# Kernel tuning notes

Measured on AMD Instinct MI355X. Metric: run time of the kernel, lower is better.

Reference implementation:

```python
import jax, jax.numpy as jnp
import numpy as np

N_NODES = 50000
N_EDGES = 800000
FEAT_DIM = 64
NUM_RELS = 8


def setup_inputs() -> dict:
    key = jax.random.key(0)
    k1, k2, k3, k4, k5 = jax.random.split(key, 5)
    features = jax.random.normal(k1, (N_NODES, FEAT_DIM), dtype=jnp.float32)
    # xavier_uniform with relu gain ~= sqrt(2)*sqrt(6/(D+D))
    limit = np.sqrt(2.0) * np.sqrt(6.0 / (FEAT_DIM + FEAT_DIM))
    weight_r = jax.random.uniform(k2, (NUM_RELS, FEAT_DIM, FEAT_DIM), dtype=jnp.float32,
                                  minval=-limit, maxval=limit)
    src = jax.random.randint(k3, (N_EDGES,), 0, N_NODES, dtype=jnp.int64 if jax.config.jax_enable_x64 else jnp.int32)
    dst = jax.random.randint(k4, (N_EDGES,), 0, N_NODES, dtype=src.dtype)
    etype = jax.random.randint(k5, (N_EDGES,), 0, NUM_RELS, dtype=src.dtype)
    return {"features": features, "weight_r": weight_r, "src": src, "dst": dst, "etype": etype}


def reference(features, weight_r, src, dst, etype):
    N, D = features.shape
    c = 0.2
    # in-degree of each destination node (DGL 'deg' node data)
    deg = jax.ops.segment_sum(jnp.ones(dst.shape, dtype=features.dtype), dst, num_segments=N)
    # relation-batched matmul: h @ W_r for every relation, then gather per edge.
    # [R, N, D] = 8*50000*64 floats -- cheap vs. materializing [E, D, D] weights.
    hw = jnp.einsum('nd,rdf->rnf', features, weight_r)
    msg = hw[etype, src] / deg[dst][:, None]          # [E, D]
    M = jax.ops.segment_sum(msg, dst, num_segments=N)  # scatter-sum mailbox reduce
    updated = jax.nn.relu(c * features + (1.0 - c) * M)
    # DGL only applies reduce to nodes that received messages; others keep h.
    return jnp.where((deg > 0)[:, None], updated, features)
```

## Files before the change

### kernel.cpp

```cpp
#include <hip/hip_runtime.h>
#include <hip/hip_bf16.h>

#define N_NODES 50000
#define N_EDGES 800000
#define FEAT 64
#define NRELS 8
#define NPB 32
#define NBUCK 1563
#define NBP 196
#define BCAP 768
#define FB_BLOCKS 782

typedef __attribute__((ext_vector_type(8))) short bf16x8;
typedef __attribute__((ext_vector_type(4))) float f32x4;

static __host__ __device__ inline size_t align256(size_t x) { return (x + 255) & ~(size_t)255; }

__device__ inline unsigned short f2b(float f) {
    unsigned u = __builtin_bit_cast(unsigned, f);
    unsigned r = (u + 0x7fffu + ((u >> 16) & 1u)) >> 16;
    return (unsigned short)r;
}
__device__ inline float b2f(unsigned short u) {
    unsigned v = ((unsigned)u) << 16;
    return __builtin_bit_cast(float, v);
}

__global__ void bfill_kernel(const int* __restrict__ dst, const int* __restrict__ srcv,
                             const int* __restrict__ et, const float* __restrict__ W,
                             const float* __restrict__ feat,
                             int* __restrict__ bcnt, int* __restrict__ tmp,
                             unsigned short* __restrict__ WtT,
                             unsigned short* __restrict__ Fb, int E, int N) {
    const int t = threadIdx.x;

    if (blockIdx.x >= NBP) {
        const int fbb = blockIdx.x - NBP;
        if (fbb < 32) {
            int i4 = fbb * 256 + t;
            float4 v = ((const float4*)W)[i4];
            int bse = i4 * 4;
            int f0 = bse & 63;
            int rd = bse >> 6;
            int d  = rd & 63;
            int r  = rd >> 6;
            unsigned short* w0 = WtT + ((size_t)(r * 64 + f0) * 64 + d);
            w0[0 * 64] = f2b(v.x);
            w0[1 * 64] = f2b(v.y);
            w0[2 * 64] = f2b(v.z);
            w0[3 * 64] = f2b(v.w);
        }
        const int node = fbb * 64 + (t >> 2);
        if (node >= N) return;
        const int seg = t & 3;
        const float4* F4 = (const float4*)feat + (size_t)node * 16 + seg * 4;
        float4 v0 = F4[0], v1 = F4[1], v2 = F4[2], v3 = F4[3];
        bf16x8 b0, b1;
        b0[0] = (short)f2b(v0.x); b0[1] = (short)f2b(v0.y);
        b0[2] = (short)f2b(v0.z); b0[3] = (short)f2b(v0.w);
        b0[4] = (short)f2b(v1.x); b0[5] = (short)f2b(v1.y);
        b0[6] = (short)f2b(v1.z); b0[7] = (short)f2b(v1.w);
        b1[0] = (short)f2b(v2.x); b1[1] = (short)f2b(v2.y);
        b1[2] = (short)f2b(v2.z); b1[3] = (short)f2b(v2.w);
        b1[4] = (short)f2b(v3.x); b1[5] = (short)f2b(v3.y);
        b1[6] = (short)f2b(v3.z); b1[7] = (short)f2b(v3.w);
        *(bf16x8*)(Fb + (size_t)node * 64 + seg * 16)     = b0;
        *(bf16x8*)(Fb + (size_t)node * 64 + seg * 16 + 8) = b1;
        return;
    }

    __shared__ int hist[NBUCK];
    __shared__ int base[NBUCK];
    __shared__ int lcur[NBUCK];
    for (int j = t; j < NBUCK; j += 256) { hist[j] = 0; lcur[j] = 0; }
    __syncthreads();

    const int4* dst4 = (const int4*)dst;
    const int4* src4 = (const int4*)srcv;
    const int4* et4  = (const int4*)et;
    const int n4 = E >> 2;
    int bk[16], pk[16];
#pragma unroll
    for (int k = 0; k < 4; k++) {
        int i4 = blockIdx.x * 1024 + t + k * 256;
        if (i4 < n4) {
            int4 d = dst4[i4];
            int4 s = src4[i4];
            int4 r = et4[i4];
            const int dd[4] = {d.x, d.y, d.z, d.w};
            const int ss[4] = {s.x, s.y, s.z, s.w};
            const int rr[4] = {r.x, r.y, r.z, r.w};
#pragma unroll
            for (int j = 0; j < 4; j++) {
                int idx = k * 4 + j;
                bk[idx] = dd[j] >> 5;
                pk[idx] = (ss[j] & 0xFFFF) | (rr[j] << 16) | ((dd[j] & 31) << 19);
                atomicAdd(&hist[bk[idx]], 1);
            }
        } else {
#pragma unroll
            for (int j = 0; j < 4; j++) bk[k * 4 + j] = -1;
        }
    }
    __syncthreads();
    for (int j = t; j < NBUCK; j += 256)
        if (hist[j] > 0)
            base[j] = j * BCAP + atomicAdd(&bcnt[j], hist[j]);
    __syncthreads();
#pragma unroll
    for (int k = 0; k < 16; k++) {
        if (bk[k] >= 0) {
            int r = atomicAdd(&lcur[bk[k]], 1);
            int pos = base[bk[k]] + r;
            if (pos < (bk[k] + 1) * BCAP)
                tmp[pos] = pk[k];
        }
    }
}

__global__ __launch_bounds__(256, 4) void fuse_kernel(
    const int* __restrict__ bcnt, const int* __restrict__ tmp,
    const unsigned short* __restrict__ Fb,
    const unsigned short* __restrict__ WtT, const float* __restrict__ feat,
    float* __restrict__ out, int N) {
    __shared__ unsigned short Sb[NRELS][NPB][64];
    __shared__ int sedge[BCAP];
    __shared__ int hist[256];
    __shared__ int noff[NPB + 1];
    __shared__ int wsum[4];
    const int t = threadIdx.x;
    const int bkt = blockIdx.x;
    const int n0 = bkt * NPB;
    const int nn = min(NPB, N - n0);
    const int gid = t >> 3, q = t & 7;

    {
        f32x4 z = {0.f, 0.f, 0.f, 0.f};
        f32x4* zp = (f32x4*)&Sb[0][0][0];
#pragma unroll
        for (int i = 0; i < 8; i++) zp[t + 256 * i] = z;
    }
    hist[t] = 0;
    __syncthreads();

    const int cnt = min(bcnt[bkt], BCAP);
    const int* tb = tmp + (size_t)bkt * BCAP;
    int v0 = (t < cnt) ? tb[t] : -1;
    int v1 = (t + 256 < cnt) ? tb[t + 256] : -1;
    int v2 = (t + 512 < cnt) ? tb[t + 512] : -1;
    if (v0 >= 0) atomicAdd(&hist[(v0 >> 16) & 255], 1);
    if (v1 >= 0) atomicAdd(&hist[(v1 >> 16) & 255], 1);
    if (v2 >= 0) atomicAdd(&hist[(v2 >> 16) & 255], 1);
    __syncthreads();
    const int myc = hist[t];
    int x = myc;
#pragma unroll
    for (int o = 1; o < 64; o <<= 1) {
        int u_ = __shfl_up(x, o);
        if ((t & 63) >= o) x += u_;
    }
    if ((t & 63) == 63) wsum[t >> 6] = x;
    __syncthreads();
    {
        int add = 0;
        const int wv = t >> 6;
        if (wv > 0) add += wsum[0];
        if (wv > 1) add += wsum[1];
        if (wv > 2) add += wsum[2];
        x += add;
    }
    const int ex = x - myc;
    if ((t & 7) == 0) noff[t >> 3] = ex;
    if (t == 255) noff[NPB] = ex + myc;
    hist[t] = ex;
    __syncthreads();
    if (v0 >= 0) { int p = atomicAdd(&hist[(v0 >> 16) & 255], 1); sedge[p] = v0; }
    if (v1 >= 0) { int p = atomicAdd(&hist[(v1 >> 16) & 255], 1); sedge[p] = v1; }
    if (v2 >= 0) { int p = atomicAdd(&hist[(v2 >> 16) & 255], 1); sedge[p] = v2; }
    __syncthreads();

    int b = 0, e = 0;
    if (gid < nn) { b = noff[gid]; e = noff[gid + 1]; }
    if (gid < nn && b < e) {
        const int swz = (q ^ (gid & 7)) * 8;
        unsigned short* srow = &Sb[0][0][0] + (size_t)gid * 64 + swz;
        float a[8] = {0.f, 0.f, 0.f, 0.f, 0.f, 0.f, 0.f, 0.f};
        int curR = -1;

        auto flushS = [&](int rel) {
            bf16x8 v;
#pragma unroll
            for (int k = 0; k < 8; k++) v[k] = (short)f2b(a[k]);
            *(bf16x8*)(srow + (size_t)rel * (NPB * 64)) = v;
        };

        int pkc[2][8];
        bf16x8 uc[2][8];
#pragma unroll
        for (int j = 0; j < 8; j++) {
            int pk = (b + j < e) ? sedge[b + j] : -1;
            pkc[0][j] = pk;
            uc[0][j] = (bf16x8){0, 0, 0, 0, 0, 0, 0, 0};
            if (pk >= 0)
                uc[0][j] = *(const bf16x8*)(Fb + (size_t)(pk & 0xFFFF) * 64 + q * 8);
        }
        __builtin_amdgcn_sched_barrier(0);
#pragma unroll
        for (int c = 0; c < 4; c++) {
            const int cur = c & 1, nxt = (c & 1) ^ 1;
            if (c < 3) {
                const int cb = b + (c + 1) * 8;
#pragma unroll
                for (int j = 0; j < 8; j++) {
                    int pk = (cb + j < e) ? sedge[cb + j] : -1;
                    pkc[nxt][j] = pk;
                    uc[nxt][j] = (bf16x8){0, 0, 0, 0, 0, 0, 0, 0};
                    if (pk >= 0)
                        uc[nxt][j] = *(const bf16x8*)(Fb + (size_t)(pk & 0xFFFF) * 64 + q * 8);
                }
            }
            __builtin_amdgcn_sched_barrier(0);
#pragma unroll
            for (int j = 0; j < 8; j++) {
                int pk = pkc[cur][j];
                if (pk >= 0) {
                    bf16x8 uu = uc[cur][j];
                    int rel = (pk >> 16) & 7;
                    if (rel != curR) {
                        if (curR >= 0) flushS(curR);
                        curR = rel;
#pragma unroll
                        for (int k = 0; k < 8; k++) a[k] = b2f((unsigned short)uu[k]);
                    } else {
#pragma unroll
                        for (int k = 0; k < 8; k++) a[k] += b2f((unsigned short)uu[k]);
                    }
                }
            }
            if (b + (c + 1) * 8 >= e) break;
        }
        for (int i = b + 32; i < e; i++) {
            int pk = sedge[i];
            bf16x8 uu = *(const bf16x8*)(Fb + (size_t)(pk & 0xFFFF) * 64 + q * 8);
            int rel = (pk >> 16) & 7;
            if (rel != curR) {
                if (curR >= 0) flushS(curR);
                curR = rel;
#pragma unroll
                for (int k = 0; k < 8; k++) a[k] = b2f((unsigned short)uu[k]);
            } else {
#pragma unroll
                for (int k = 0; k < 8; k++) a[k] += b2f((unsigned short)uu[k]);
            }
        }
        if (curR >= 0) flushS(curR);
    }

    float4 h0e = make_float4(0.f, 0.f, 0.f, 0.f), h1e = h0e;
    const int ef0 = q * 8;
    if (gid < nn) {
        const float4* fp = (const float4*)feat + (size_t)(n0 + gid) * 16 + (ef0 >> 2);
        h0e = fp[0];
        h1e = fp[1];
    }
    __syncthreads();

    const int w = t >> 6, l = t & 63, col = l & 15, quad = l >> 4;
    f32x4 acc0 = {0.f, 0.f, 0.f, 0.f}, acc1 = {0.f, 0.f, 0.f, 0.f};
    const int sw0 = (quad ^ (col & 7)) * 8;
    const int sw1 = ((quad + 4) ^ (col & 7)) * 8;
#pragma unroll
    for (int r = 0; r < NRELS; r++) {
        const unsigned short* wp = WtT + (size_t)r * 4096 + ((w * 16 + col) * 64 + quad * 8);
        bf16x8 b0 = *(const bf16x8*)wp;
        bf16x8 b1 = *(const bf16x8*)(wp + 32);
        const unsigned short* Sr = &Sb[0][0][0] + (size_t)r * (NPB * 64);
        bf16x8 a0 = *(const bf16x8*)&Sr[col * 64 + sw0];
        bf16x8 a1 = *(const bf16x8*)&Sr[col * 64 + sw1];
        bf16x8 c0 = *(const bf16x8*)&Sr[(16 + col) * 64 + sw0];
        bf16x8 c1 = *(const bf16x8*)&Sr[(16 + col) * 64 + sw1];
        acc0 = __builtin_amdgcn_mfma_f32_16x16x32_bf16(a0, b0, acc0, 0, 0, 0);
        acc0 = __builtin_amdgcn_mfma_f32_16x16x32_bf16(a1, b1, acc0, 0, 0, 0);
        acc1 = __builtin_amdgcn_mfma_f32_16x16x32_bf16(c0, b0, acc1, 0, 0, 0);
        acc1 = __builtin_amdgcn_mfma_f32_16x16x32_bf16(c1, b1, acc1, 0, 0, 0);
    }
    __syncthreads();

    float* C = (float*)&Sb[0][0][0];
#pragma unroll
    for (int i = 0; i < 4; i++) {
        C[(quad * 4 + i) * 72 + w * 16 + col]        = acc0[i];
        C[(16 + quad * 4 + i) * 72 + w * 16 + col]   = acc1[i];
    }
    __syncthreads();

    if (gid < nn) {
        const int gn = n0 + gid;
        const int deg = e - b;
        float4 m0 = *(const float4*)&C[gid * 72 + ef0];
        float4 m1 = *(const float4*)&C[gid * 72 + ef0 + 4];
        float4 r0, r1;
        if (deg > 0) {
            float inv = 0.8f / (float)deg;
            r0.x = fmaxf(0.2f * h0e.x + m0.x * inv, 0.f);
            r0.y = fmaxf(0.2f * h0e.y + m0.y * inv, 0.f);
            r0.z = fmaxf(0.2f * h0e.z + m0.z * inv, 0.f);
            r0.w = fmaxf(0.2f * h0e.w + m0.w * inv, 0.f);
            r1.x = fmaxf(0.2f * h1e.x + m1.x * inv, 0.f);
            r1.y = fmaxf(0.2f * h1e.y + m1.y * inv, 0.f);
            r1.z = fmaxf(0.2f * h1e.z + m1.z * inv, 0.f);
            r1.w = fmaxf(0.2f * h1e.w + m1.w * inv, 0.f);
        } else {
            r0 = h0e; r1 = h1e;
        }
        float4* op = (float4*)out + (size_t)gn * 16 + (ef0 >> 2);
        op[0] = r0;
        op[1] = r1;
    }
}

__global__ void degf_kernel(const int* __restrict__ dst, float* __restrict__ deg, int E) {
    int e = blockIdx.x * blockDim.x + threadIdx.x;
    if (e < E) atomicAdd(deg + dst[e], 1.0f);
}

__global__ void otf_kernel(const int* __restrict__ src, const int* __restrict__ dst,
                           const int* __restrict__ et, const float* __restrict__ feat,
                           const float* __restrict__ W, float* __restrict__ out, int E) {
    int wid = (blockIdx.x * blockDim.x + threadIdx.x) >> 6;
    int l = threadIdx.x & 63;
    if (wid >= E) return;
    int s = src[wid], dd = dst[wid], r = et[wid];
    float fv = feat[(size_t)s * 64 + l];
    const float* Wr = W + (size_t)r * 4096;
    float acc = 0.f;
#pragma unroll
    for (int d = 0; d < 64; d++) {
        float a = __shfl(fv, d);
        acc += a * Wr[d * 64 + l];
    }
    atomicAdd(out + (size_t)dd * 64 + l, acc);
}

__global__ void final_kernel(const float* __restrict__ feat, const float* __restrict__ deg,
                             float* __restrict__ out, int N) {
    int i = blockIdx.x * blockDim.x + threadIdx.x;
    if (i >= N * 16) return;
    int n = i >> 4;
    float d = deg[n];
    float4 f = ((const float4*)feat)[i];
    float4 m = ((float4*)out)[i];
    float4 res;
    if (d > 0.f) {
        float inv = 0.8f / d;
        res.x = fmaxf(0.2f * f.x + m.x * inv, 0.f);
        res.y = fmaxf(0.2f * f.y + m.y * inv, 0.f);
        res.z = fmaxf(0.2f * f.z + m.z * inv, 0.f);
        res.w = fmaxf(0.2f * f.w + m.w * inv, 0.f);
    } else {
        res = f;
    }
    ((float4*)out)[i] = res;
}

extern "C" void kernel_launch(void* const* d_in, const int* in_sizes, int n_in,
                              void* d_out, int out_size, void* d_ws, size_t ws_size,
                              hipStream_t stream) {
    const float* feat = (const float*)d_in[0];
    const float* W    = (const float*)d_in[1];
    const int*   src  = (const int*)d_in[2];
    const int*   dst  = (const int*)d_in[3];
    const int*   et   = (const int*)d_in[4];
    float* out = (float*)d_out;

    const int N = N_NODES, E = N_EDGES;

    char* p = (char*)d_ws;
    int* bcnt  = (int*)p;  p += align256((size_t)NBUCK * 4);
    int* tmp   = (int*)p;  p += align256((size_t)NBUCK * BCAP * 4);
    unsigned short* WtT = (unsigned short*)p;
    p += align256((size_t)NRELS * FEAT * FEAT * 2);
    unsigned short* Fb = (unsigned short*)p;
    p += align256((size_t)N * FEAT * 2);
    size_t need_full = (size_t)(p - (char*)d_ws);

    if (ws_size >= need_full) {
        hipMemsetAsync(bcnt, 0, (size_t)NBUCK * 4, stream);
        bfill_kernel<<<NBP + FB_BLOCKS, 256, 0, stream>>>(dst, src, et, W, feat,
                                                          bcnt, tmp, WtT, Fb, E, N);
        fuse_kernel<<<NBUCK, 256, 0, stream>>>(bcnt, tmp, Fb, WtT, feat, out, N);
    } else {
        float* deg = (float*)d_ws;
        hipMemsetAsync(out, 0, (size_t)N * FEAT * 4, stream);
        hipMemsetAsync(deg, 0, (size_t)N * 4, stream);
        degf_kernel<<<(E + 255) / 256, 256, 0, stream>>>(dst, deg, E);
        otf_kernel<<<(E + 3) / 4, 256, 0, stream>>>(src, dst, et, feat, W, out, E);
        final_kernel<<<(N * 16 + 255) / 256, 256, 0, stream>>>(feat, deg, out, N);
    }
}
```

Baseline: 124.0 us.

## Merge bucket-fill and fuse kernels into one persistent kernel with grid barrier

```diff
diff --git a/kernel.cpp b/kernel.cpp
--- a/kernel.cpp
+++ b/kernel.cpp
@@ -7,9 +7,9 @@
 #define NRELS 8
 #define NPB 32
 #define NBUCK 1563
-#define NBP 196
 #define BCAP 768
-#define FB_BLOCKS 782
+#define NBLK 1024
+#define SMEM_BYTES 37024
 
 typedef __attribute__((ext_vector_type(8))) short bf16x8;
 typedef __attribute__((ext_vector_type(4))) float f32x4;
@@ -26,20 +26,49 @@
     return __builtin_bit_cast(float, v);
 }
 
-__global__ void bfill_kernel(const int* __restrict__ dst, const int* __restrict__ srcv,
-                             const int* __restrict__ et, const float* __restrict__ W,
-                             const float* __restrict__ feat,
-                             int* __restrict__ bcnt, int* __restrict__ tmp,
-                             unsigned short* __restrict__ WtT,
-                             unsigned short* __restrict__ Fb, int E, int N) {
+__global__ __launch_bounds__(256, 4) void mega_kernel(
+    const int* __restrict__ dst, const int* __restrict__ srcv,
+    const int* __restrict__ et, const float* __restrict__ W,
+    const float* __restrict__ feat,
+    int* __restrict__ bcnt, int* bar, int* __restrict__ tmp,
+    unsigned short* __restrict__ WtT, unsigned short* __restrict__ Fb,
+    float* __restrict__ out, int E, int N) {
+    __shared__ __attribute__((aligned(16))) unsigned char smem[SMEM_BYTES];
     const int t = threadIdx.x;
-
-    if (blockIdx.x >= NBP) {
-        const int fbb = blockIdx.x - NBP;
-        if (fbb < 32) {
-            int i4 = fbb * 256 + t;
-            float4 v = ((const float4*)W)[i4];
-            int bse = i4 * 4;
+    const int bid = blockIdx.x;
+
+    {
+        int* histA = (int*)smem;
+        int* baseA = histA + NBUCK;
+        int* lcurA = baseA + NBUCK;
+        for (int j = t; j < NBUCK; j += 256) { histA[j] = 0; lcurA[j] = 0; }
+        __syncthreads();
+
+        const int n4 = E >> 2;
+        const int i4 = bid * 196 + t;
+        int bk[4], pk[4];
+        if (t < 196 && i4 < n4) {
+            int4 d = ((const int4*)dst)[i4];
+            int4 s = ((const int4*)srcv)[i4];
+            int4 r = ((const int4*)et)[i4];
+            const int dd[4] = {d.x, d.y, d.z, d.w};
+            const int ss[4] = {s.x, s.y, s.z, s.w};
+            const int rr[4] = {r.x, r.y, r.z, r.w};
+#pragma unroll
+            for (int j = 0; j < 4; j++) {
+                bk[j] = dd[j] >> 5;
+                pk[j] = (ss[j] & 0xFFFF) | (rr[j] << 16) | ((dd[j] & 31) << 19);
+                atomicAdd(&histA[bk[j]], 1);
+            }
+        } else {
+#pragma unroll
+            for (int j = 0; j < 4; j++) bk[j] = -1;
+        }
+
+        if (t < 8) {
+            int i4w = bid * 8 + t;
+            float4 v = ((const float4*)W)[i4w];
+            int bse = i4w * 4;
             int f0 = bse & 63;
             int rd = bse >> 6;
             int d  = rd & 63;
@@ -50,272 +79,250 @@
             w0[2 * 64] = f2b(v.z);
             w0[3 * 64] = f2b(v.w);
         }
-        const int node = fbb * 64 + (t >> 2);
-        if (node >= N) return;
-        const int seg = t & 3;
-        const float4* F4 = (const float4*)feat + (size_t)node * 16 + seg * 4;
-        float4 v0 = F4[0], v1 = F4[1], v2 = F4[2], v3 = F4[3];
-        bf16x8 b0, b1;
-        b0[0] = (short)f2b(v0.x); b0[1] = (short)f2b(v0.y);
-        b0[2] = (short)f2b(v0.z); b0[3] = (short)f2b(v0.w);
-        b0[4] = (short)f2b(v1.x); b0[5] = (short)f2b(v1.y);
-        b0[6] = (short)f2b(v1.z); b0[7] = (short)f2b(v1.w);
-        b1[0] = (short)f2b(v2.x); b1[1] = (short)f2b(v2.y);
-        b1[2] = (short)f2b(v2.z); b1[3] = (short)f2b(v2.w);
-        b1[4] = (short)f2b(v3.x); b1[5] = (short)f2b(v3.y);
-        b1[6] = (short)f2b(v3.z); b1[7] = (short)f2b(v3.w);
-        *(bf16x8*)(Fb + (size_t)node * 64 + seg * 16)     = b0;
-        *(bf16x8*)(Fb + (size_t)node * 64 + seg * 16 + 8) = b1;
-        return;
-    }
-
-    __shared__ int hist[NBUCK];
-    __shared__ int base[NBUCK];
-    __shared__ int lcur[NBUCK];
-    for (int j = t; j < NBUCK; j += 256) { hist[j] = 0; lcur[j] = 0; }
+
+        {
+            const int idx = bid * 196 + t;
+            const int node = idx >> 2;
+            if (t < 196 && node < N) {
+                const int seg = idx & 3;
+                const float4* F4 = (const float4*)feat + (size_t)node * 16 + seg * 4;
+                float4 v0 = F4[0], v1 = F4[1], v2 = F4[2], v3 = F4[3];
+                bf16x8 b0, b1;
+                b0[0] = (short)f2b(v0.x); b0[1] = (short)f2b(v0.y);
+                b0[2] = (short)f2b(v0.z); b0[3] = (short)f2b(v0.w);
+                b0[4] = (short)f2b(v1.x); b0[5] = (short)f2b(v1.y);
+                b0[6] = (short)f2b(v1.z); b0[7] = (short)f2b(v1.w);
+                b1[0] = (short)f2b(v2.x); b1[1] = (short)f2b(v2.y);
+                b1[2] = (short)f2b(v2.z); b1[3] = (short)f2b(v2.w);
+                b1[4] = (short)f2b(v3.x); b1[5] = (short)f2b(v3.y);
+                b1[6] = (short)f2b(v3.z); b1[7] = (short)f2b(v3.w);
+                *(bf16x8*)(Fb + (size_t)node * 64 + seg * 16)     = b0;
+                *(bf16x8*)(Fb + (size_t)node * 64 + seg * 16 + 8) = b1;
+            }
+        }
+        __syncthreads();
+        for (int j = t; j < NBUCK; j += 256)
+            if (histA[j] > 0)
+                baseA[j] = j * BCAP + atomicAdd(&bcnt[j], histA[j]);
+        __syncthreads();
+#pragma unroll
+        for (int j = 0; j < 4; j++) {
+            if (bk[j] >= 0) {
+                int r = atomicAdd(&lcurA[bk[j]], 1);
+                int pos = baseA[bk[j]] + r;
+                if (pos < (bk[j] + 1) * BCAP)
+                    tmp[pos] = pk[j];
+            }
+        }
+    }
+
     __syncthreads();
-
-    const int4* dst4 = (const int4*)dst;
-    const int4* src4 = (const int4*)srcv;
-    const int4* et4  = (const int4*)et;
-    const int n4 = E >> 2;
-    int bk[16], pk[16];
-#pragma unroll
-    for (int k = 0; k < 4; k++) {
-        int i4 = blockIdx.x * 1024 + t + k * 256;
-        if (i4 < n4) {
-            int4 d = dst4[i4];
-            int4 s = src4[i4];
-            int4 r = et4[i4];
-            const int dd[4] = {d.x, d.y, d.z, d.w};
-            const int ss[4] = {s.x, s.y, s.z, s.w};
-            const int rr[4] = {r.x, r.y, r.z, r.w};
-#pragma unroll
-            for (int j = 0; j < 4; j++) {
-                int idx = k * 4 + j;
-                bk[idx] = dd[j] >> 5;
-                pk[idx] = (ss[j] & 0xFFFF) | (rr[j] << 16) | ((dd[j] & 31) << 19);
-                atomicAdd(&hist[bk[idx]], 1);
-            }
-        } else {
-#pragma unroll
-            for (int j = 0; j < 4; j++) bk[k * 4 + j] = -1;
-        }
+    __threadfence();
+    if (t == 0) {
+        __hip_atomic_fetch_add(bar, 1, __ATOMIC_ACQ_REL, __HIP_MEMORY_SCOPE_AGENT);
+        while (__hip_atomic_load(bar, __ATOMIC_ACQUIRE, __HIP_MEMORY_SCOPE_AGENT) < NBLK)
+            __builtin_amdgcn_s_sleep(16);
     }
     __syncthreads();
-    for (int j = t; j < NBUCK; j += 256)
-        if (hist[j] > 0)
-            base[j] = j * BCAP + atomicAdd(&bcnt[j], hist[j]);
-    __syncthreads();
-#pragma unroll
-    for (int k = 0; k < 16; k++) {
-        if (bk[k] >= 0) {
-            int r = atomicAdd(&lcur[bk[k]], 1);
-            int pos = base[bk[k]] + r;
-            if (pos < (bk[k] + 1) * BCAP)
-                tmp[pos] = pk[k];
-        }
-    }
-}
-
-__global__ __launch_bounds__(256, 4) void fuse_kernel(
-    const int* __restrict__ bcnt, const int* __restrict__ tmp,
-    const unsigned short* __restrict__ Fb,
-    const unsigned short* __restrict__ WtT, const float* __restrict__ feat,
-    float* __restrict__ out, int N) {
-    __shared__ unsigned short Sb[NRELS][NPB][64];
-    __shared__ int sedge[BCAP];
-    __shared__ int hist[256];
-    __shared__ int noff[NPB + 1];
-    __shared__ int wsum[4];
-    const int t = threadIdx.x;
-    const int bkt = blockIdx.x;
-    const int n0 = bkt * NPB;
-    const int nn = min(NPB, N - n0);
+    __threadfence();
+
+    unsigned short* Sb = (unsigned short*)smem;
+    int* sedge = (int*)(smem + 32768);
+    int* histC = (int*)(smem + 32768 + 3072);
+    int* noff  = (int*)(smem + 36864);
+    int* wsum  = (int*)(smem + 36996);
     const int gid = t >> 3, q = t & 7;
 
-    {
-        f32x4 z = {0.f, 0.f, 0.f, 0.f};
-        f32x4* zp = (f32x4*)&Sb[0][0][0];
-#pragma unroll
-        for (int i = 0; i < 8; i++) zp[t + 256 * i] = z;
-    }
-    hist[t] = 0;
-    __syncthreads();
-
-    const int cnt = min(bcnt[bkt], BCAP);
-    const int* tb = tmp + (size_t)bkt * BCAP;
-    int v0 = (t < cnt) ? tb[t] : -1;
-    int v1 = (t + 256 < cnt) ? tb[t + 256] : -1;
-    int v2 = (t + 512 < cnt) ? tb[t + 512] : -1;
-    if (v0 >= 0) atomicAdd(&hist[(v0 >> 16) & 255], 1);
-    if (v1 >= 0) atomicAdd(&hist[(v1 >> 16) & 255], 1);
-    if (v2 >= 0) atomicAdd(&hist[(v2 >> 16) & 255], 1);
-    __syncthreads();
-    const int myc = hist[t];
-    int x = myc;
-#pragma unroll
-    for (int o = 1; o < 64; o <<= 1) {
-        int u_ = __shfl_up(x, o);
-        if ((t & 63) >= o) x += u_;
-    }
-    if ((t & 63) == 63) wsum[t >> 6] = x;
-    __syncthreads();
-    {
-        int add = 0;
-        const int wv = t >> 6;
-        if (wv > 0) add += wsum[0];
-        if (wv > 1) add += wsum[1];
-        if (wv > 2) add += wsum[2];
-        x += add;
-    }
-    const int ex = x - myc;
-    if ((t & 7) == 0) noff[t >> 3] = ex;
-    if (t == 255) noff[NPB] = ex + myc;
-    hist[t] = ex;
-    __syncthreads();
-    if (v0 >= 0) { int p = atomicAdd(&hist[(v0 >> 16) & 255], 1); sedge[p] = v0; }
-    if (v1 >= 0) { int p = atomicAdd(&hist[(v1 >> 16) & 255], 1); sedge[p] = v1; }
-    if (v2 >= 0) { int p = atomicAdd(&hist[(v2 >> 16) & 255], 1); sedge[p] = v2; }
-    __syncthreads();
-
-    int b = 0, e = 0;
-    if (gid < nn) { b = noff[gid]; e = noff[gid + 1]; }
-    if (gid < nn && b < e) {
-        const int swz = (q ^ (gid & 7)) * 8;
-        unsigned short* srow = &Sb[0][0][0] + (size_t)gid * 64 + swz;
-        float a[8] = {0.f, 0.f, 0.f, 0.f, 0.f, 0.f, 0.f, 0.f};
-        int curR = -1;
-
-        auto flushS = [&](int rel) {
-            bf16x8 v;
-#pragma unroll
-            for (int k = 0; k < 8; k++) v[k] = (short)f2b(a[k]);
-            *(bf16x8*)(srow + (size_t)rel * (NPB * 64)) = v;
-        };
-
-        int pkc[2][8];
-        bf16x8 uc[2][8];
-#pragma unroll
-        for (int j = 0; j < 8; j++) {
-            int pk = (b + j < e) ? sedge[b + j] : -1;
-            pkc[0][j] = pk;
-            uc[0][j] = (bf16x8){0, 0, 0, 0, 0, 0, 0, 0};
-            if (pk >= 0)
-                uc[0][j] = *(const bf16x8*)(Fb + (size_t)(pk & 0xFFFF) * 64 + q * 8);
-        }
-        __builtin_amdgcn_sched_barrier(0);
-#pragma unroll
-        for (int c = 0; c < 4; c++) {
-            const int cur = c & 1, nxt = (c & 1) ^ 1;
-            if (c < 3) {
-                const int cb = b + (c + 1) * 8;
+    for (int bkt = bid; bkt < NBUCK; bkt += NBLK) {
+        __syncthreads();
+        const int n0 = bkt * NPB;
+        const int nn = min(NPB, N - n0);
+
+        {
+            f32x4 z = {0.f, 0.f, 0.f, 0.f};
+            f32x4* zp = (f32x4*)Sb;
+#pragma unroll
+            for (int i = 0; i < 8; i++) zp[t + 256 * i] = z;
+        }
+        histC[t] = 0;
+        __syncthreads();
+
+        const int cnt = min(bcnt[bkt], BCAP);
+        const int* tb = tmp + (size_t)bkt * BCAP;
+        int v0 = (t < cnt) ? tb[t] : -1;
+        int v1 = (t + 256 < cnt) ? tb[t + 256] : -1;
+        int v2 = (t + 512 < cnt) ? tb[t + 512] : -1;
+        if (v0 >= 0) atomicAdd(&histC[(v0 >> 16) & 255], 1);
+        if (v1 >= 0) atomicAdd(&histC[(v1 >> 16) & 255], 1);
+        if (v2 >= 0) atomicAdd(&histC[(v2 >> 16) & 255], 1);
+        __syncthreads();
+        const int myc = histC[t];
+        int x = myc;
+#pragma unroll
+        for (int o = 1; o < 64; o <<= 1) {
+            int u_ = __shfl_up(x, o);
+            if ((t & 63) >= o) x += u_;
+        }
+        if ((t & 63) == 63) wsum[t >> 6] = x;
+        __syncthreads();
+        {
+            int add = 0;
+            const int wv = t >> 6;
+            if (wv > 0) add += wsum[0];
+            if (wv > 1) add += wsum[1];
+            if (wv > 2) add += wsum[2];
+            x += add;
+        }
+        const int ex = x - myc;
+        if ((t & 7) == 0) noff[t >> 3] = ex;
+        if (t == 255) noff[NPB] = ex + myc;
+        histC[t] = ex;
+        __syncthreads();
+        if (v0 >= 0) { int p = atomicAdd(&histC[(v0 >> 16) & 255], 1); sedge[p] = v0; }
+        if (v1 >= 0) { int p = atomicAdd(&histC[(v1 >> 16) & 255], 1); sedge[p] = v1; }
+        if (v2 >= 0) { int p = atomicAdd(&histC[(v2 >> 16) & 255], 1); sedge[p] = v2; }
+        __syncthreads();
+
+        int b = 0, e = 0;
+        if (gid < nn) { b = noff[gid]; e = noff[gid + 1]; }
+        if (gid < nn && b < e) {
+            const int swz = (q ^ (gid & 7)) * 8;
+            unsigned short* srow = Sb + (size_t)gid * 64 + swz;
+            float a[8] = {0.f, 0.f, 0.f, 0.f, 0.f, 0.f, 0.f, 0.f};
+            int curR = -1;
+
+            auto flushS = [&](int rel) {
+                bf16x8 v;
+#pragma unroll
+                for (int k = 0; k < 8; k++) v[k] = (short)f2b(a[k]);
+                *(bf16x8*)(srow + (size_t)rel * (NPB * 64)) = v;
+            };
+            auto issue = [&](int cb, int (&pk)[8], bf16x8 (&u)[8]) {
 #pragma unroll
                 for (int j = 0; j < 8; j++) {
-                    int pk = (cb + j < e) ? sedge[cb + j] : -1;
-                    pkc[nxt][j] = pk;
-                    uc[nxt][j] = (bf16x8){0, 0, 0, 0, 0, 0, 0, 0};
-                    if (pk >= 0)
-                        uc[nxt][j] = *(const bf16x8*)(Fb + (size_t)(pk & 0xFFFF) * 64 + q * 8);
+                    int p = (cb + j < e) ? sedge[cb + j] : -1;
+                    pk[j] = p;
+                    u[j] = (bf16x8){0, 0, 0, 0, 0, 0, 0, 0};
+                    if (p >= 0)
+                        u[j] = *(const bf16x8*)(Fb + (size_t)(p & 0xFFFF) * 64 + q * 8);
                 }
-            }
-            __builtin_amdgcn_sched_barrier(0);
-#pragma unroll
-            for (int j = 0; j < 8; j++) {
-                int pk = pkc[cur][j];
-                if (pk >= 0) {
-                    bf16x8 uu = uc[cur][j];
-                    int rel = (pk >> 16) & 7;
-                    if (rel != curR) {
-                        if (curR >= 0) flushS(curR);
-                        curR = rel;
-#pragma unroll
-                        for (int k = 0; k < 8; k++) a[k] = b2f((unsigned short)uu[k]);
-                    } else {
-#pragma unroll
-                        for (int k = 0; k < 8; k++) a[k] += b2f((unsigned short)uu[k]);
+            };
+            auto consume = [&](int (&pk)[8], bf16x8 (&u)[8]) {
+#pragma unroll
+                for (int j = 0; j < 8; j++) {
+                    int p = pk[j];
+                    if (p >= 0) {
+                        bf16x8 uu = u[j];
+                        int rel = (p >> 16) & 7;
+                        if (rel != curR) {
+                            if (curR >= 0) flushS(curR);
+                            curR = rel;
+#pragma unroll
+                            for (int k = 0; k < 8; k++) a[k] = b2f((unsigned short)uu[k]);
+                        } else {
+#pragma unroll
+                            for (int k = 0; k < 8; k++) a[k] += b2f((unsigned short)uu[k]);
+                        }
                     }
                 }
-            }
-            if (b + (c + 1) * 8 >= e) break;
-        }
-        for (int i = b + 32; i < e; i++) {
-            int pk = sedge[i];
-            bf16x8 uu = *(const bf16x8*)(Fb + (size_t)(pk & 0xFFFF) * 64 + q * 8);
-            int rel = (pk >> 16) & 7;
-            if (rel != curR) {
-                if (curR >= 0) flushS(curR);
-                curR = rel;
-#pragma unroll
-                for (int k = 0; k < 8; k++) a[k] = b2f((unsigned short)uu[k]);
+            };
+
+            int pkA[8], pkB[8];
+            bf16x8 uA[8], uB[8];
+            issue(b, pkA, uA);
+            __builtin_amdgcn_sched_barrier(0);
+            if (b + 8 < e) issue(b + 8, pkB, uB);
+            __builtin_amdgcn_sched_barrier(0);
+            consume(pkA, uA);
+            if (b + 8 < e) {
+                if (b + 16 < e) issue(b + 16, pkA, uA);
+                __builtin_amdgcn_sched_barrier(0);
+                consume(pkB, uB);
+                if (b + 16 < e) {
+                    if (b + 24 < e) issue(b + 24, pkB, uB);
+                    __builtin_amdgcn_sched_barrier(0);
+                    consume(pkA, uA);
+                    if (b + 24 < e) consume(pkB, uB);
+                }
+            }
+            for (int i = b + 32; i < e; i++) {
+                int p = sedge[i];
+                bf16x8 uu = *(const bf16x8*)(Fb + (size_t)(p & 0xFFFF) * 64 + q * 8);
+                int rel = (p >> 16) & 7;
+                if (rel != curR) {
+                    if (curR >= 0) flushS(curR);
+                    curR = rel;
+#pragma unroll
+                    for (int k = 0; k < 8; k++) a[k] = b2f((unsigned short)uu[k]);
+                } else {
+#pragma unroll
+                    for (int k = 0; k < 8; k++) a[k] += b2f((unsigned short)uu[k]);
+                }
+            }
+            if (curR >= 0) flushS(curR);
+        }
+
+        float4 h0e = make_float4(0.f, 0.f, 0.f, 0.f), h1e = h0e;
+        const int ef0 = q * 8;
+        if (gid < nn) {
+            const float4* fp = (const float4*)feat + (size_t)(n0 + gid) * 16 + (ef0 >> 2);
+            h0e = fp[0];
+            h1e = fp[1];
+        }
+        __syncthreads();
+
+        const int w = t >> 6, l = t & 63, col = l & 15, quad = l >> 4;
+        f32x4 acc0 = {0.f, 0.f, 0.f, 0.f}, acc1 = {0.f, 0.f, 0.f, 0.f};
+        const int sw0 = (quad ^ (col & 7)) * 8;
+        const int sw1 = ((quad + 4) ^ (col & 7)) * 8;
+#pragma unroll
+        for (int r = 0; r < NRELS; r++) {
+            const unsigned short* wp = WtT + (size_t)r * 4096 + ((w * 16 + col) * 64 + quad * 8);
+            bf16x8 b0 = *(const bf16x8*)wp;
+            bf16x8 b1 = *(const bf16x8*)(wp + 32);
+            const unsigned short* Sr = Sb + (size_t)r * (NPB * 64);
+            bf16x8 a0 = *(const bf16x8*)&Sr[col * 64 + sw0];
+            bf16x8 a1 = *(const bf16x8*)&Sr[col * 64 + sw1];
+            bf16x8 c0 = *(const bf16x8*)&Sr[(16 + col) * 64 + sw0];
+            bf16x8 c1 = *(const bf16x8*)&Sr[(16 + col) * 64 + sw1];
+            acc0 = __builtin_amdgcn_mfma_f32_16x16x32_bf16(a0, b0, acc0, 0, 0, 0);
+            acc0 = __builtin_amdgcn_mfma_f32_16x16x32_bf16(a1, b1, acc0, 0, 0, 0);
+            acc1 = __builtin_amdgcn_mfma_f32_16x16x32_bf16(c0, b0, acc1, 0, 0, 0);
+            acc1 = __builtin_amdgcn_mfma_f32_16x16x32_bf16(c1, b1, acc1, 0, 0, 0);
+        }
+        __syncthreads();
+
+        float* C = (float*)Sb;
+#pragma unroll
+        for (int i = 0; i < 4; i++) {
+            C[(quad * 4 + i) * 72 + w * 16 + col]      = acc0[i];
+            C[(16 + quad * 4 + i) * 72 + w * 16 + col] = acc1[i];
+        }
+        __syncthreads();
+
+        if (gid < nn) {
+            const int gn = n0 + gid;
+            const int deg = e - b;
+            float4 m0 = *(const float4*)&C[gid * 72 + ef0];
+            float4 m1 = *(const float4*)&C[gid * 72 + ef0 + 4];
+            float4 r0, r1;
+            if (deg > 0) {
+                float inv = 0.8f / (float)deg;
+                r0.x = fmaxf(0.2f * h0e.x + m0.x * inv, 0.f);
+                r0.y = fmaxf(0.2f * h0e.y + m0.y * inv, 0.f);
+                r0.z = fmaxf(0.2f * h0e.z + m0.z * inv, 0.f);
+                r0.w = fmaxf(0.2f * h0e.w + m0.w * inv, 0.f);
+                r1.x = fmaxf(0.2f * h1e.x + m1.x * inv, 0.f);
+                r1.y = fmaxf(0.2f * h1e.y + m1.y * inv, 0.f);
+                r1.z = fmaxf(0.2f * h1e.z + m1.z * inv, 0.f);
+                r1.w = fmaxf(0.2f * h1e.w + m1.w * inv, 0.f);
             } else {
-#pragma unroll
-                for (int k = 0; k < 8; k++) a[k] += b2f((unsigned short)uu[k]);
-            }
-        }
-        if (curR >= 0) flushS(curR);
-    }
-
-    float4 h0e = make_float4(0.f, 0.f, 0.f, 0.f), h1e = h0e;
-    const int ef0 = q * 8;
-    if (gid < nn) {
-        const float4* fp = (const float4*)feat + (size_t)(n0 + gid) * 16 + (ef0 >> 2);
-        h0e = fp[0];
-        h1e = fp[1];
-    }
-    __syncthreads();
-
-    const int w = t >> 6, l = t & 63, col = l & 15, quad = l >> 4;
-    f32x4 acc0 = {0.f, 0.f, 0.f, 0.f}, acc1 = {0.f, 0.f, 0.f, 0.f};
-    const int sw0 = (quad ^ (col & 7)) * 8;
-    const int sw1 = ((quad + 4) ^ (col & 7)) * 8;
-#pragma unroll
-    for (int r = 0; r < NRELS; r++) {
-        const unsigned short* wp = WtT + (size_t)r * 4096 + ((w * 16 + col) * 64 + quad * 8);
-        bf16x8 b0 = *(const bf16x8*)wp;
-        bf16x8 b1 = *(const bf16x8*)(wp + 32);
-        const unsigned short* Sr = &Sb[0][0][0] + (size_t)r * (NPB * 64);
-        bf16x8 a0 = *(const bf16x8*)&Sr[col * 64 + sw0];
-        bf16x8 a1 = *(const bf16x8*)&Sr[col * 64 + sw1];
-        bf16x8 c0 = *(const bf16x8*)&Sr[(16 + col) * 64 + sw0];
-        bf16x8 c1 = *(const bf16x8*)&Sr[(16 + col) * 64 + sw1];
-        acc0 = __builtin_amdgcn_mfma_f32_16x16x32_bf16(a0, b0, acc0, 0, 0, 0);
-        acc0 = __builtin_amdgcn_mfma_f32_16x16x32_bf16(a1, b1, acc0, 0, 0, 0);
-        acc1 = __builtin_amdgcn_mfma_f32_16x16x32_bf16(c0, b0, acc1, 0, 0, 0);
-        acc1 = __builtin_amdgcn_mfma_f32_16x16x32_bf16(c1, b1, acc1, 0, 0, 0);
-    }
-    __syncthreads();
-
-    float* C = (float*)&Sb[0][0][0];
-#pragma unroll
-    for (int i = 0; i < 4; i++) {
-        C[(quad * 4 + i) * 72 + w * 16 + col]        = acc0[i];
-        C[(16 + quad * 4 + i) * 72 + w * 16 + col]   = acc1[i];
-    }
-    __syncthreads();
-
-    if (gid < nn) {
-        const int gn = n0 + gid;
-        const int deg = e - b;
-        float4 m0 = *(const float4*)&C[gid * 72 + ef0];
-        float4 m1 = *(const float4*)&C[gid * 72 + ef0 + 4];
-        float4 r0, r1;
-        if (deg > 0) {
-            float inv = 0.8f / (float)deg;
-            r0.x = fmaxf(0.2f * h0e.x + m0.x * inv, 0.f);
-            r0.y = fmaxf(0.2f * h0e.y + m0.y * inv, 0.f);
-            r0.z = fmaxf(0.2f * h0e.z + m0.z * inv, 0.f);
-            r0.w = fmaxf(0.2f * h0e.w + m0.w * inv, 0.f);
-            r1.x = fmaxf(0.2f * h1e.x + m1.x * inv, 0.f);
-            r1.y = fmaxf(0.2f * h1e.y + m1.y * inv, 0.f);
-            r1.z = fmaxf(0.2f * h1e.z + m1.z * inv, 0.f);
-            r1.w = fmaxf(0.2f * h1e.w + m1.w * inv, 0.f);
-        } else {
-            r0 = h0e; r1 = h1e;
-        }
-        float4* op = (float4*)out + (size_t)gn * 16 + (ef0 >> 2);
-        op[0] = r0;
-        op[1] = r1;
+                r0 = h0e; r1 = h1e;
+            }
+            float4* op = (float4*)out + (size_t)gn * 16 + (ef0 >> 2);
+            op[0] = r0;
+            op[1] = r1;
+        }
     }
 }
 
@@ -376,8 +383,10 @@
     const int N = N_NODES, E = N_EDGES;
 
     char* p = (char*)d_ws;
-    int* bcnt  = (int*)p;  p += align256((size_t)NBUCK * 4);
-    int* tmp   = (int*)p;  p += align256((size_t)NBUCK * BCAP * 4);
+    int* bcnt = (int*)p;
+    int* bar  = bcnt + NBUCK;
+    p += align256((size_t)(NBUCK + 1) * 4);
+    int* tmp  = (int*)p;  p += align256((size_t)NBUCK * BCAP * 4);
     unsigned short* WtT = (unsigned short*)p;
     p += align256((size_t)NRELS * FEAT * FEAT * 2);
     unsigned short* Fb = (unsigned short*)p;
@@ -385,10 +394,9 @@
     size_t need_full = (size_t)(p - (char*)d_ws);
 
     if (ws_size >= need_full) {
-        hipMemsetAsync(bcnt, 0, (size_t)NBUCK * 4, stream);
-        bfill_kernel<<<NBP + FB_BLOCKS, 256, 0, stream>>>(dst, src, et, W, feat,
-                                                          bcnt, tmp, WtT, Fb, E, N);
-        fuse_kernel<<<NBUCK, 256, 0, stream>>>(bcnt, tmp, Fb, WtT, feat, out, N);
+        hipMemsetAsync(bcnt, 0, (size_t)(NBUCK + 1) * 4, stream);
+        mega_kernel<<<NBLK, 256, 0, stream>>>(dst, src, et, W, feat,
+                                              bcnt, bar, tmp, WtT, Fb, out, E, N);
     } else {
         float* deg = (float*)d_ws;
         hipMemsetAsync(out, 0, (size_t)N * FEAT * 4, stream);
```

New measurement: 494.0 us. +298.3%, slower.
